# Performance work log

Measured on AMD Instinct MI355X. Metric: run time of the kernel, lower is better.

Reference implementation:

```python
import jax, jax.numpy as jnp
import numpy as np

N_NODES = 100000
N_EDGES = 3200000
IN_F = 128
HID = 32


def setup_inputs() -> dict:
    key = jax.random.key(0)
    k = jax.random.split(key, 8)
    x = jax.random.normal(k[0], (N_NODES, IN_F), dtype=jnp.float32)
    edge_index = jax.random.randint(k[1], (2, N_EDGES), 0, N_NODES, dtype=jnp.int64)
    edge_weight = jax.random.uniform(k[2], (N_EDGES,), dtype=jnp.float32)
    # GCN conv weight (in -> 32) and bias, then Linear(32 -> 1)
    s1 = 1.0 / np.sqrt(IN_F)
    s2 = 1.0 / np.sqrt(HID)
    W1 = jax.random.uniform(k[3], (IN_F, HID), dtype=jnp.float32, minval=-s1, maxval=s1)
    b1 = jax.random.uniform(k[4], (HID,), dtype=jnp.float32, minval=-s1, maxval=s1)
    W2 = jax.random.uniform(k[5], (HID, 1), dtype=jnp.float32, minval=-s2, maxval=s2)
    b2 = jax.random.uniform(k[6], (1,), dtype=jnp.float32, minval=-s2, maxval=s2)
    return {"x": x, "edge_index": edge_index, "edge_weight": edge_weight,
            "W1": W1, "b1": b1, "W2": W2, "b2": b2}


def gcn_conv(x, edge_index, edge_weight, W, b):
    N = x.shape[0]
    src = edge_index[0]
    dst = edge_index[1]
    loop = jnp.arange(N, dtype=edge_index.dtype)
    row = jnp.concatenate([dst, loop])  # aggregation targets
    col = jnp.concatenate([src, loop])  # message sources
    w = jnp.concatenate([edge_weight, jnp.ones((N,), dtype=x.dtype)])
    deg = jax.ops.segment_sum(w, row, num_segments=N)
    dinv = jnp.where(deg > 0, deg ** -0.5, 0.0).astype(x.dtype)
    norm = dinv[row] * w * dinv[col]  # [E+N]
    h = x @ W  # [N, 32]  transform before gather (cheaper)
    msgs = norm[:, None] * h[col]  # [E+N, 32]
    agg = jax.ops.segment_sum(msgs, row, num_segments=N)  # [N, 32]
    return agg + b


def reference(x, edge_index, edge_weight, W1, b1, W2, b2):
    h = gcn_conv(x, edge_index, edge_weight, W1, b1)
    h = jax.nn.relu(h)
    return h @ W2 + b2  # [N, 1]
```

## Files before the change

kernel.cpp:

```cpp
#include <hip/hip_runtime.h>
#include <hip/hip_bf16.h>
#include <hip/hip_fp16.h>

#define NN 100000
#define NE 3200000
#define IN_F 128
#define HID 32

#define BNODES 131
#define NB 764
#define NBP1 (NB + 1)
#define PBLK 768
#define EPB 4168
#define SSPAN 4736

typedef __hip_bfloat16 bf16;
typedef __attribute__((ext_vector_type(8))) short s16x8;
typedef __attribute__((ext_vector_type(4))) float f32x4;

__global__ __launch_bounds__(512) void k_part(const int* __restrict__ ei,
                                              const float* __restrict__ ew,
                                              int* __restrict__ offs,
                                              uint2* __restrict__ raw) {
    __shared__ int hist[NB];
    __shared__ int start[NB];
    __shared__ int wtot8[8];
    __shared__ __align__(16) uint2 sp[EPB];

    int t = threadIdx.x;
    int blk = blockIdx.x;
    for (int b = t; b < NB; b += 512) hist[b] = 0;
    __syncthreads();

    unsigned pk[10]; unsigned wb[10]; int bkt[10];
    int base_e = blk * EPB;
#pragma unroll
    for (int j = 0; j < 5; j++) {
        int p = j * 512 + t;
        int e = base_e + 2 * p;
        bool v = (p < (EPB / 2)) && (e < NE);
        if (v) {
            int2   s2 = *(const int2*)(ei + e);
            int2   d2 = *(const int2*)(ei + NE + e);
            float2 w2 = *(const float2*)(ew + e);
            int bk0 = d2.x / BNODES;
            bkt[2 * j]     = bk0;
            pk[2 * j]      = (unsigned)s2.x | ((unsigned)(d2.x - bk0 * BNODES) << 20);
            wb[2 * j]      = __float_as_uint(w2.x);
            int bk1 = d2.y / BNODES;
            bkt[2 * j + 1] = bk1;
            pk[2 * j + 1]  = (unsigned)s2.y | ((unsigned)(d2.y - bk1 * BNODES) << 20);
            wb[2 * j + 1]  = __float_as_uint(w2.y);
        } else { bkt[2 * j] = -1; bkt[2 * j + 1] = -1; }
    }
#pragma unroll
    for (int j = 0; j < 10; j++)
        if (bkt[j] >= 0) atomicAdd(&hist[bkt[j]], 1);
    __syncthreads();

    int e0 = 2 * t, e1 = 2 * t + 1;
    int h0 = (e0 < NB) ? hist[e0] : 0;
    int h1 = (e1 < NB) ? hist[e1] : 0;
    int psum = h0 + h1;
    int lane = t & 63;
    int incl = psum;
#pragma unroll
    for (int off = 1; off < 64; off <<= 1) {
        int up = __shfl_up(incl, off, 64);
        if (lane >= off) incl += up;
    }
    int wid = t >> 6;
    if (lane == 63) wtot8[wid] = incl;
    __syncthreads();
    int woff = 0;
    for (int wj = 0; wj < wid; wj++) woff += wtot8[wj];
    int exc = woff + incl - psum;
    if (e0 < NB) start[e0] = exc;
    if (e1 < NB) start[e1] = exc + h0;
    __syncthreads();

    int total = start[NB - 1] + hist[NB - 1];
    int* orow = offs + (size_t)blk * NBP1;
    for (int b = t; b < NB; b += 512) orow[b] = start[b];
    if (t == 0) orow[NB] = total;
    __syncthreads();

#pragma unroll
    for (int j = 0; j < 10; j++) {
        if (bkt[j] >= 0) {
            int pos = atomicAdd(&start[bkt[j]], 1);
            sp[pos] = make_uint2(pk[j], wb[j]);
        }
    }
    __syncthreads();

    uint2* r = raw + (size_t)blk * EPB;
    int tot2 = total >> 1;
    const uint4* sp4 = (const uint4*)sp;
    uint4* r4 = (uint4*)r;
    for (int i = t; i < tot2; i += 512) r4[i] = sp4[i];
    if (t == 0 && (total & 1)) r[total - 1] = sp[total - 1];
}

__global__ __launch_bounds__(256) void k_trans(const int* __restrict__ in, int* __restrict__ out) {
    __shared__ int tile[32][33];
    int c0 = blockIdx.x * 32, r0 = blockIdx.y * 32;
    int tx = threadIdx.x & 31, ty = threadIdx.x >> 5;
    for (int i = ty; i < 32; i += 8) {
        int r = r0 + i, c = c0 + tx;
        if (r < PBLK && c < NBP1) tile[i][tx] = in[(size_t)r * NBP1 + c];
    }
    __syncthreads();
    for (int i = ty; i < 32; i += 8) {
        int c = c0 + i, r = r0 + tx;
        if (c < NBP1 && r < PBLK) out[(size_t)c * PBLK + r] = tile[tx][i];
    }
}

__global__ __launch_bounds__(512) void k_dh(const int* __restrict__ offsT,
                                            const uint2* __restrict__ raw,
                                            const float* __restrict__ x,
                                            const float* __restrict__ W1,
                                            float* __restrict__ dinv,
                                            bf16* __restrict__ hs) {
    __shared__ unsigned short runid[SSPAN];
    __shared__ int P[PBLK + 1];
    __shared__ int basearr[PBLK];
    __shared__ float wsumf[BNODES];
    __shared__ float dinvl[BNODES];
    __shared__ int wt8[8];

    int t = threadIdx.x;
    int b = blockIdx.x;
    if (t < BNODES) wsumf[t] = 0.f;

    int e0 = 2 * t, e1 = 2 * t + 1;
    int l0 = 0, l1 = 0, o0v = 0, o1v = 0;
    if (e0 < PBLK) {
        o0v = offsT[(size_t)b * PBLK + e0];
        l0  = offsT[(size_t)(b + 1) * PBLK + e0] - o0v;
    }
    if (e1 < PBLK) {
        o1v = offsT[(size_t)b * PBLK + e1];
        l1  = offsT[(size_t)(b + 1) * PBLK + e1] - o1v;
    }
    int psum = l0 + l1;
    int lane = t & 63;
    int incl = psum;
#pragma unroll
    for (int off = 1; off < 64; off <<= 1) {
        int up = __shfl_up(incl, off, 64);
        if (lane >= off) incl += up;
    }
    int wid = t >> 6;
    if (lane == 63) wt8[wid] = incl;
    __syncthreads();
    int woff = 0;
    for (int wj = 0; wj < wid; wj++) woff += wt8[wj];
    int exc = woff + incl - psum;
    if (e0 < PBLK) { P[e0] = exc;      basearr[e0] = o0v - exc; }
    if (e1 < PBLK) { P[e1] = exc + l0; basearr[e1] = o1v - (exc + l0); }
    if (t == 0) {
        int s = 0;
#pragma unroll
        for (int j = 0; j < 8; j++) s += wt8[j];
        P[PBLK] = s;
    }
    __syncthreads();

    int total = min(P[PBLK], SSPAN);

    for (int r = t; r < PBLK; r += 512) {
        int p0 = P[r], p1 = min(P[r + 1], SSPAN);
        for (int i = p0; i < p1; i++) runid[i] = (unsigned short)r;
    }
    __syncthreads();

#pragma unroll
    for (int k = 0; k < 10; k++) {
        int d = t + k * 512;
        if (d < total) {
            int r = runid[d];
            uint2 rec = raw[(size_t)r * EPB + (basearr[r] + d)];
            atomicAdd(&wsumf[(rec.x >> 20) & 255], __uint_as_float(rec.y));
        }
    }
    __syncthreads();

    if (t < BNODES) {
        float dv = rsqrtf(wsumf[t] + 1.0f);
        dinvl[t] = dv;
        int node = b * BNODES + t;
        if (node < NN) dinv[node] = dv;
    }
    __syncthreads();

    int wv = t >> 6;
    int m = lane & 15;
    int q = lane >> 4;

    s16x8 wf[8];
    {
#pragma unroll
        for (int ks2 = 0; ks2 < 4; ks2++) {
#pragma unroll
            for (int nt = 0; nt < 2; nt++) {
                union { s16x8 v; unsigned short u[8]; } wu;
#pragma unroll
                for (int j = 0; j < 8; j++) {
                    int kk = ks2 * 32 + q * 8 + j;
                    __hip_bfloat16 bv = __float2bfloat16(W1[kk * HID + m + 16 * nt]);
                    wu.u[j] = *(unsigned short*)&bv;
                }
                wf[ks2 * 2 + nt] = wu.v;
            }
        }
    }

    for (int tile = wv; tile * 16 < BNODES; tile += 8) {
        int lrow = tile * 16 + m;
        int node = b * BNODES + lrow;
        bool valid = (lrow < BNODES) && (node < NN);

        f32x4 acc0 = {0.f, 0.f, 0.f, 0.f};
        f32x4 acc1 = {0.f, 0.f, 0.f, 0.f};
        const float* rowp = x + (size_t)node * IN_F + q * 8;

#pragma unroll
        for (int ks = 0; ks < 4; ks++) {
            float4 f0 = {0,0,0,0}, f1 = {0,0,0,0};
            if (valid) {
                const float4* xr = (const float4*)(rowp + ks * 32);
                f0 = xr[0]; f1 = xr[1];
            }
            union { s16x8 v; unsigned u32[4]; } af;
            __hip_bfloat162 p0 = __float22bfloat162_rn({f0.x, f0.y});
            __hip_bfloat162 p1 = __float22bfloat162_rn({f0.z, f0.w});
            __hip_bfloat162 p2 = __float22bfloat162_rn({f1.x, f1.y});
            __hip_bfloat162 p3 = __float22bfloat162_rn({f1.z, f1.w});
            af.u32[0] = *(unsigned*)&p0;
            af.u32[1] = *(unsigned*)&p1;
            af.u32[2] = *(unsigned*)&p2;
            af.u32[3] = *(unsigned*)&p3;
            acc0 = __builtin_amdgcn_mfma_f32_16x16x32_bf16(af.v, wf[ks * 2 + 0], acc0, 0, 0, 0);
            acc1 = __builtin_amdgcn_mfma_f32_16x16x32_bf16(af.v, wf[ks * 2 + 1], acc1, 0, 0, 0);
        }

        int f = m;
#pragma unroll
        for (int r = 0; r < 4; r++) {
            int l2 = tile * 16 + q * 4 + r;
            int n2 = b * BNODES + l2;
            if (l2 < BNODES && n2 < NN) {
                float dv = dinvl[l2];
                hs[(size_t)n2 * HID + f]      = __float2bfloat16(dv * acc0[r]);
                hs[(size_t)n2 * HID + f + 16] = __float2bfloat16(dv * acc1[r]);
            }
        }
    }
}

__global__ __launch_bounds__(512) void k_agg(const int* __restrict__ offsT,
                                             const uint2* __restrict__ raw,
                                             const bf16* __restrict__ hs,
                                             const float* __restrict__ dinv,
                                             const float* __restrict__ b1, const float* __restrict__ W2,
                                             const float* __restrict__ b2, float* __restrict__ out) {
    __shared__ uint2 se[SSPAN];
    __shared__ int P[PBLK + 1];
    __shared__ int basearr[PBLK];
    __shared__ int hist[BNODES];
    __shared__ int scanbuf[BNODES];
    __shared__ int cur[BNODES];
    __shared__ int wt8[8];

    unsigned short* runid = (unsigned short*)se;

    int t = threadIdx.x;
    int b = blockIdx.x;
    if (t < BNODES) hist[t] = 0;

    int e0 = 2 * t, e1 = 2 * t + 1;
    int l0 = 0, l1 = 0, o0v = 0, o1v = 0;
    if (e0 < PBLK) {
        o0v = offsT[(size_t)b * PBLK + e0];
        l0  = offsT[(size_t)(b + 1) * PBLK + e0] - o0v;
    }
    if (e1 < PBLK) {
        o1v = offsT[(size_t)b * PBLK + e1];
        l1  = offsT[(size_t)(b + 1) * PBLK + e1] - o1v;
    }
    int psum = l0 + l1;
    int lane = t & 63;
    int incl = psum;
#pragma unroll
    for (int off = 1; off < 64; off <<= 1) {
        int up = __shfl_up(incl, off, 64);
        if (lane >= off) incl += up;
    }
    int wid = t >> 6;
    if (lane == 63) wt8[wid] = incl;
    __syncthreads();
    int woff = 0;
    for (int wj = 0; wj < wid; wj++) woff += wt8[wj];
    int exc = woff + incl - psum;
    if (e0 < PBLK) { P[e0] = exc;      basearr[e0] = o0v - exc; }
    if (e1 < PBLK) { P[e1] = exc + l0; basearr[e1] = o1v - (exc + l0); }
    if (t == 0) {
        int s = 0;
#pragma unroll
        for (int j = 0; j < 8; j++) s += wt8[j];
        P[PBLK] = s;
    }
    __syncthreads();

    int total = min(P[PBLK], SSPAN);

    for (int r = t; r < PBLK; r += 512) {
        int p0 = P[r], p1 = min(P[r + 1], SSPAN);
        for (int i = p0; i < p1; i++) runid[i] = (unsigned short)r;
    }
    __syncthreads();

    uint2 rr[10];
#pragma unroll
    for (int k = 0; k < 10; k++) {
        int d = t + k * 512;
        if (d < total) {
            int r = runid[d];
            uint2 rec = raw[(size_t)r * EPB + (basearr[r] + d)];
            rr[k] = rec;
            int dl = (rec.x >> 20) & 255;
            atomicAdd(&hist[dl], 1);
        }
    }
    __syncthreads();

    if (t < BNODES) scanbuf[t] = hist[t];
    __syncthreads();
    for (int off = 1; off < BNODES; off <<= 1) {
        int v = 0;
        if (t < BNODES && t >= off) v = scanbuf[t - off];
        __syncthreads();
        if (t < BNODES) scanbuf[t] += v;
        __syncthreads();
    }
    if (t < BNODES) cur[t] = scanbuf[t] - hist[t];
    __syncthreads();

#pragma unroll
    for (int k = 0; k < 10; k++) {
        int d = t + k * 512;
        if (d < total) {
            uint2 rec = rr[k];
            int dl = (rec.x >> 20) & 255;
            int pos = atomicAdd(&cur[dl], 1);
            se[pos] = make_uint2(rec.x & 0xFFFFF, rec.y);
        }
    }
    __syncthreads();

    int gid = t >> 4;
    int l = t & 15;
    const __hip_bfloat162* hs2 = (const __hip_bfloat162*)hs;
    for (int dl = gid; dl < BNODES; dl += 32) {
        int cnt = hist[dl];
        int rs = scanbuf[dl] - cnt;
        float a0 = 0.f, a1 = 0.f;
        int full = cnt & ~7;
        int bse = 0;
        for (; bse < full; bse += 8) {
            uint2 q0 = se[rs + bse + 0];
            uint2 q1 = se[rs + bse + 1];
            uint2 q2 = se[rs + bse + 2];
            uint2 q3 = se[rs + bse + 3];
            uint2 q4 = se[rs + bse + 4];
            uint2 q5 = se[rs + bse + 5];
            uint2 q6 = se[rs + bse + 6];
            uint2 q7 = se[rs + bse + 7];
            __hip_bfloat162 h0 = hs2[(size_t)q0.x * 16 + l];
            __hip_bfloat162 h1 = hs2[(size_t)q1.x * 16 + l];
            __hip_bfloat162 h2 = hs2[(size_t)q2.x * 16 + l];
            __hip_bfloat162 h3 = hs2[(size_t)q3.x * 16 + l];
            __hip_bfloat162 h4 = hs2[(size_t)q4.x * 16 + l];
            __hip_bfloat162 h5 = hs2[(size_t)q5.x * 16 + l];
            __hip_bfloat162 h6 = hs2[(size_t)q6.x * 16 + l];
            __hip_bfloat162 h7 = hs2[(size_t)q7.x * 16 + l];
            float2 f0 = __bfloat1622float2(h0); a0 += __uint_as_float(q0.y) * f0.x; a1 += __uint_as_float(q0.y) * f0.y;
            float2 f1 = __bfloat1622float2(h1); a0 += __uint_as_float(q1.y) * f1.x; a1 += __uint_as_float(q1.y) * f1.y;
            float2 f2 = __bfloat1622float2(h2); a0 += __uint_as_float(q2.y) * f2.x; a1 += __uint_as_float(q2.y) * f2.y;
            float2 f3 = __bfloat1622float2(h3); a0 += __uint_as_float(q3.y) * f3.x; a1 += __uint_as_float(q3.y) * f3.y;
            float2 f4 = __bfloat1622float2(h4); a0 += __uint_as_float(q4.y) * f4.x; a1 += __uint_as_float(q4.y) * f4.y;
            float2 f5 = __bfloat1622float2(h5); a0 += __uint_as_float(q5.y) * f5.x; a1 += __uint_as_float(q5.y) * f5.y;
            float2 f6 = __bfloat1622float2(h6); a0 += __uint_as_float(q6.y) * f6.x; a1 += __uint_as_float(q6.y) * f6.y;
            float2 f7 = __bfloat1622float2(h7); a0 += __uint_as_float(q7.y) * f7.x; a1 += __uint_as_float(q7.y) * f7.y;
        }
        if (bse < cnt) {
            int rem = cnt - bse;
            uint2 q0 = se[rs + bse];
            uint2 q1 = se[rs + bse + (rem > 1 ? 1 : 0)];
            uint2 q2 = se[rs + bse + (rem > 2 ? 2 : 0)];
            uint2 q3 = se[rs + bse + (rem > 3 ? 3 : 0)];
            uint2 q4 = se[rs + bse + (rem > 4 ? 4 : 0)];
            uint2 q5 = se[rs + bse + (rem > 5 ? 5 : 0)];
            uint2 q6 = se[rs + bse + (rem > 6 ? 6 : 0)];
            float w0 = __uint_as_float(q0.y);
            float w1 = rem > 1 ? __uint_as_float(q1.y) : 0.f;
            float w2 = rem > 2 ? __uint_as_float(q2.y) : 0.f;
            float w3 = rem > 3 ? __uint_as_float(q3.y) : 0.f;
            float w4 = rem > 4 ? __uint_as_float(q4.y) : 0.f;
            float w5 = rem > 5 ? __uint_as_float(q5.y) : 0.f;
            float w6 = rem > 6 ? __uint_as_float(q6.y) : 0.f;
            __hip_bfloat162 h0 = hs2[(size_t)q0.x * 16 + l];
            __hip_bfloat162 h1 = hs2[(size_t)q1.x * 16 + l];
            __hip_bfloat162 h2 = hs2[(size_t)q2.x * 16 + l];
            __hip_bfloat162 h3 = hs2[(size_t)q3.x * 16 + l];
            __hip_bfloat162 h4 = hs2[(size_t)q4.x * 16 + l];
            __hip_bfloat162 h5 = hs2[(size_t)q5.x * 16 + l];
            __hip_bfloat162 h6 = hs2[(size_t)q6.x * 16 + l];
            float2 f0 = __bfloat1622float2(h0); a0 += w0 * f0.x; a1 += w0 * f0.y;
            float2 f1 = __bfloat1622float2(h1); a0 += w1 * f1.x; a1 += w1 * f1.y;
            float2 f2 = __bfloat1622float2(h2); a0 += w2 * f2.x; a1 += w2 * f2.y;
            float2 f3 = __bfloat1622float2(h3); a0 += w3 * f3.x; a1 += w3 * f3.y;
            float2 f4 = __bfloat1622float2(h4); a0 += w4 * f4.x; a1 += w4 * f4.y;
            float2 f5 = __bfloat1622float2(h5); a0 += w5 * f5.x; a1 += w5 * f5.y;
            float2 f6 = __bfloat1622float2(h6); a0 += w6 * f6.x; a1 += w6 * f6.y;
        }
        int node = b * BNODES + dl;
        if (node < NN) {
            float dv = dinv[node];
            float2 fs = __bfloat1622float2(hs2[(size_t)node * 16 + l]);
            float v0 = dv * (a0 + fs.x) + b1[2 * l];
            float v1 = dv * (a1 + fs.y) + b1[2 * l + 1];
            v0 = fmaxf(v0, 0.f);
            v1 = fmaxf(v1, 0.f);
            float ps = v0 * W2[2 * l] + v1 * W2[2 * l + 1];
#pragma unroll
            for (int m2 = 8; m2 >= 1; m2 >>= 1) ps += __shfl_xor(ps, m2, 16);
            if (l == 0) out[node] = ps + b2[0];
        }
    }
}

extern "C" void kernel_launch(void* const* d_in, const int* in_sizes, int n_in,
                              void* d_out, int out_size, void* d_ws, size_t ws_size,
                              hipStream_t stream) {
    const float* x  = (const float*)d_in[0];
    const int*   ei = (const int*)d_in[1];
    const float* ew = (const float*)d_in[2];
    const float* W1 = (const float*)d_in[3];
    const float* b1 = (const float*)d_in[4];
    const float* W2 = (const float*)d_in[5];
    const float* b2 = (const float*)d_in[6];
    float* out = (float*)d_out;

    char* ws = (char*)d_ws;
    uint2* raw   = (uint2*)(ws + 0);
    int*   offs  = (int*)  (ws + 25608192);
    int*   offsT = (int*)  (ws + 27958272);
    bf16*  hs    = (bf16*) (ws + 30308352);
    float* dinv  = (float*)(ws + 36708352);

    k_part<<<PBLK, 512, 0, stream>>>(ei, ew, offs, raw);
    k_trans<<<dim3((NBP1 + 31) / 32, (PBLK + 31) / 32), 256, 0, stream>>>(offs, offsT);
    k_dh<<<NB, 512, 0, stream>>>(offsT, raw, x, W1, dinv, hs);
    k_agg<<<NB, 512, 0, stream>>>(offsT, raw, hs, dinv, b1, W2, b2, out);
}
```

Before: 199.9 us.

## Split hidden features into two half-planes and aggregate each in a separate pass

Stores the transformed bf16 feature table as two separate planes of 16 features each, and runs the gather-aggregate loop twice, once per plane. Each pass gathers 32-byte rows instead of 64-byte rows, so each pass touches a 3.2 MB table that fits in cache better. The cost is reading the edge list from shared memory twice, doubling gather instructions with narrower 2-byte loads, and keeping a partial output sum in shared memory.

```diff
diff --git a/kernel.cpp b/kernel.cpp
--- a/kernel.cpp
+++ b/kernel.cpp
@@ -17,6 +17,10 @@
 typedef __hip_bfloat16 bf16;
 typedef __attribute__((ext_vector_type(8))) short s16x8;
 typedef __attribute__((ext_vector_type(4))) float f32x4;
+
+__device__ __forceinline__ float bf2f(unsigned short u) {
+    return __uint_as_float((unsigned)u << 16);
+}
 
 __global__ __launch_bounds__(512) void k_part(const int* __restrict__ ei,
                                               const float* __restrict__ ew,
@@ -253,8 +257,8 @@
             int n2 = b * BNODES + l2;
             if (l2 < BNODES && n2 < NN) {
                 float dv = dinvl[l2];
-                hs[(size_t)n2 * HID + f]      = __float2bfloat16(dv * acc0[r]);
-                hs[(size_t)n2 * HID + f + 16] = __float2bfloat16(dv * acc1[r]);
+                hs[(size_t)n2 * 16 + f]        = __float2bfloat16(dv * acc0[r]);
+                hs[(size_t)(NN + n2) * 16 + f] = __float2bfloat16(dv * acc1[r]);
             }
         }
     }
@@ -272,6 +276,7 @@
     __shared__ int hist[BNODES];
     __shared__ int scanbuf[BNODES];
     __shared__ int cur[BNODES];
+    __shared__ float pspart[BNODES];
     __shared__ int wt8[8];
 
     unsigned short* runid = (unsigned short*)se;
@@ -362,82 +367,80 @@
 
     int gid = t >> 4;
     int l = t & 15;
-    const __hip_bfloat162* hs2 = (const __hip_bfloat162*)hs;
-    for (int dl = gid; dl < BNODES; dl += 32) {
-        int cnt = hist[dl];
-        int rs = scanbuf[dl] - cnt;
-        float a0 = 0.f, a1 = 0.f;
-        int full = cnt & ~7;
-        int bse = 0;
-        for (; bse < full; bse += 8) {
-            uint2 q0 = se[rs + bse + 0];
-            uint2 q1 = se[rs + bse + 1];
-            uint2 q2 = se[rs + bse + 2];
-            uint2 q3 = se[rs + bse + 3];
-            uint2 q4 = se[rs + bse + 4];
-            uint2 q5 = se[rs + bse + 5];
-            uint2 q6 = se[rs + bse + 6];
-            uint2 q7 = se[rs + bse + 7];
-            __hip_bfloat162 h0 = hs2[(size_t)q0.x * 16 + l];
-            __hip_bfloat162 h1 = hs2[(size_t)q1.x * 16 + l];
-            __hip_bfloat162 h2 = hs2[(size_t)q2.x * 16 + l];
-            __hip_bfloat162 h3 = hs2[(size_t)q3.x * 16 + l];
-            __hip_bfloat162 h4 = hs2[(size_t)q4.x * 16 + l];
-            __hip_bfloat162 h5 = hs2[(size_t)q5.x * 16 + l];
-            __hip_bfloat162 h6 = hs2[(size_t)q6.x * 16 + l];
-            __hip_bfloat162 h7 = hs2[(size_t)q7.x * 16 + l];
-            float2 f0 = __bfloat1622float2(h0); a0 += __uint_as_float(q0.y) * f0.x; a1 += __uint_as_float(q0.y) * f0.y;
-            float2 f1 = __bfloat1622float2(h1); a0 += __uint_as_float(q1.y) * f1.x; a1 += __uint_as_float(q1.y) * f1.y;
-            float2 f2 = __bfloat1622float2(h2); a0 += __uint_as_float(q2.y) * f2.x; a1 += __uint_as_float(q2.y) * f2.y;
-            float2 f3 = __bfloat1622float2(h3); a0 += __uint_as_float(q3.y) * f3.x; a1 += __uint_as_float(q3.y) * f3.y;
-            float2 f4 = __bfloat1622float2(h4); a0 += __uint_as_float(q4.y) * f4.x; a1 += __uint_as_float(q4.y) * f4.y;
-            float2 f5 = __bfloat1622float2(h5); a0 += __uint_as_float(q5.y) * f5.x; a1 += __uint_as_float(q5.y) * f5.y;
-            float2 f6 = __bfloat1622float2(h6); a0 += __uint_as_float(q6.y) * f6.x; a1 += __uint_as_float(q6.y) * f6.y;
-            float2 f7 = __bfloat1622float2(h7); a0 += __uint_as_float(q7.y) * f7.x; a1 += __uint_as_float(q7.y) * f7.y;
-        }
-        if (bse < cnt) {
-            int rem = cnt - bse;
-            uint2 q0 = se[rs + bse];
-            uint2 q1 = se[rs + bse + (rem > 1 ? 1 : 0)];
-            uint2 q2 = se[rs + bse + (rem > 2 ? 2 : 0)];
-            uint2 q3 = se[rs + bse + (rem > 3 ? 3 : 0)];
-            uint2 q4 = se[rs + bse + (rem > 4 ? 4 : 0)];
-            uint2 q5 = se[rs + bse + (rem > 5 ? 5 : 0)];
-            uint2 q6 = se[rs + bse + (rem > 6 ? 6 : 0)];
-            float w0 = __uint_as_float(q0.y);
-            float w1 = rem > 1 ? __uint_as_float(q1.y) : 0.f;
-            float w2 = rem > 2 ? __uint_as_float(q2.y) : 0.f;
-            float w3 = rem > 3 ? __uint_as_float(q3.y) : 0.f;
-            float w4 = rem > 4 ? __uint_as_float(q4.y) : 0.f;
-            float w5 = rem > 5 ? __uint_as_float(q5.y) : 0.f;
-            float w6 = rem > 6 ? __uint_as_float(q6.y) : 0.f;
-            __hip_bfloat162 h0 = hs2[(size_t)q0.x * 16 + l];
-            __hip_bfloat162 h1 = hs2[(size_t)q1.x * 16 + l];
-            __hip_bfloat162 h2 = hs2[(size_t)q2.x * 16 + l];
-            __hip_bfloat162 h3 = hs2[(size_t)q3.x * 16 + l];
-            __hip_bfloat162 h4 = hs2[(size_t)q4.x * 16 + l];
-            __hip_bfloat162 h5 = hs2[(size_t)q5.x * 16 + l];
-            __hip_bfloat162 h6 = hs2[(size_t)q6.x * 16 + l];
-            float2 f0 = __bfloat1622float2(h0); a0 += w0 * f0.x; a1 += w0 * f0.y;
-            float2 f1 = __bfloat1622float2(h1); a0 += w1 * f1.x; a1 += w1 * f1.y;
-            float2 f2 = __bfloat1622float2(h2); a0 += w2 * f2.x; a1 += w2 * f2.y;
-            float2 f3 = __bfloat1622float2(h3); a0 += w3 * f3.x; a1 += w3 * f3.y;
-            float2 f4 = __bfloat1622float2(h4); a0 += w4 * f4.x; a1 += w4 * f4.y;
-            float2 f5 = __bfloat1622float2(h5); a0 += w5 * f5.x; a1 += w5 * f5.y;
-            float2 f6 = __bfloat1622float2(h6); a0 += w6 * f6.x; a1 += w6 * f6.y;
-        }
-        int node = b * BNODES + dl;
-        if (node < NN) {
-            float dv = dinv[node];
-            float2 fs = __bfloat1622float2(hs2[(size_t)node * 16 + l]);
-            float v0 = dv * (a0 + fs.x) + b1[2 * l];
-            float v1 = dv * (a1 + fs.y) + b1[2 * l + 1];
-            v0 = fmaxf(v0, 0.f);
-            v1 = fmaxf(v1, 0.f);
-            float ps = v0 * W2[2 * l] + v1 * W2[2 * l + 1];
-#pragma unroll
-            for (int m2 = 8; m2 >= 1; m2 >>= 1) ps += __shfl_xor(ps, m2, 16);
-            if (l == 0) out[node] = ps + b2[0];
+    const unsigned short* hsu = (const unsigned short*)hs;
+#pragma unroll
+    for (int h = 0; h < 2; h++) {
+        const unsigned short* hsh = hsu + (size_t)h * NN * 16;
+        for (int dl = gid; dl < BNODES; dl += 32) {
+            int cnt = hist[dl];
+            int rs = scanbuf[dl] - cnt;
+            float a = 0.f;
+            int full = cnt & ~7;
+            int bse = 0;
+            for (; bse < full; bse += 8) {
+                uint2 q0 = se[rs + bse + 0];
+                uint2 q1 = se[rs + bse + 1];
+                uint2 q2 = se[rs + bse + 2];
+                uint2 q3 = se[rs + bse + 3];
+                uint2 q4 = se[rs + bse + 4];
+                uint2 q5 = se[rs + bse + 5];
+                uint2 q6 = se[rs + bse + 6];
+                uint2 q7 = se[rs + bse + 7];
+                float h0 = bf2f(hsh[(size_t)q0.x * 16 + l]);
+                float h1 = bf2f(hsh[(size_t)q1.x * 16 + l]);
+                float h2 = bf2f(hsh[(size_t)q2.x * 16 + l]);
+                float h3 = bf2f(hsh[(size_t)q3.x * 16 + l]);
+                float h4 = bf2f(hsh[(size_t)q4.x * 16 + l]);
+                float h5 = bf2f(hsh[(size_t)q5.x * 16 + l]);
+                float h6 = bf2f(hsh[(size_t)q6.x * 16 + l]);
+                float h7 = bf2f(hsh[(size_t)q7.x * 16 + l]);
+                a += __uint_as_float(q0.y) * h0;
+                a += __uint_as_float(q1.y) * h1;
+                a += __uint_as_float(q2.y) * h2;
+                a += __uint_as_float(q3.y) * h3;
+                a += __uint_as_float(q4.y) * h4;
+                a += __uint_as_float(q5.y) * h5;
+                a += __uint_as_float(q6.y) * h6;
+                a += __uint_as_float(q7.y) * h7;
+            }
+            if (bse < cnt) {
+                int rem = cnt - bse;
+                uint2 q0 = se[rs + bse];
+                uint2 q1 = se[rs + bse + (rem > 1 ? 1 : 0)];
+                uint2 q2 = se[rs + bse + (rem > 2 ? 2 : 0)];
+                uint2 q3 = se[rs + bse + (rem > 3 ? 3 : 0)];
+                uint2 q4 = se[rs + bse + (rem > 4 ? 4 : 0)];
+                uint2 q5 = se[rs + bse + (rem > 5 ? 5 : 0)];
+                uint2 q6 = se[rs + bse + (rem > 6 ? 6 : 0)];
+                float w0 = __uint_as_float(q0.y);
+                float w1 = rem > 1 ? __uint_as_float(q1.y) : 0.f;
+                float w2 = rem > 2 ? __uint_as_float(q2.y) : 0.f;
+                float w3 = rem > 3 ? __uint_as_float(q3.y) : 0.f;
+                float w4 = rem > 4 ? __uint_as_float(q4.y) : 0.f;
+                float w5 = rem > 5 ? __uint_as_float(q5.y) : 0.f;
+                float w6 = rem > 6 ? __uint_as_float(q6.y) : 0.f;
+                a += w0 * bf2f(hsh[(size_t)q0.x * 16 + l]);
+                a += w1 * bf2f(hsh[(size_t)q1.x * 16 + l]);
+                a += w2 * bf2f(hsh[(size_t)q2.x * 16 + l]);
+                a += w3 * bf2f(hsh[(size_t)q3.x * 16 + l]);
+                a += w4 * bf2f(hsh[(size_t)q4.x * 16 + l]);
+                a += w5 * bf2f(hsh[(size_t)q5.x * 16 + l]);
+                a += w6 * bf2f(hsh[(size_t)q6.x * 16 + l]);
+            }
+            int node = b * BNODES + dl;
+            if (node < NN) {
+                float dv = dinv[node];
+                float fs = bf2f(hsh[(size_t)node * 16 + l]);
+                float v = dv * (a + fs) + b1[h * 16 + l];
+                v = fmaxf(v, 0.f);
+                float ps = v * W2[h * 16 + l];
+#pragma unroll
+                for (int m2 = 8; m2 >= 1; m2 >>= 1) ps += __shfl_xor(ps, m2, 16);
+                if (l == 0) {
+                    if (h == 0) pspart[dl] = ps;
+                    else        out[node] = ps + pspart[dl] + b2[0];
+                }
+            }
         }
     }
 }
```

Result: slower. 211.4 us (+5.7%).
